# Kernel optimization log

Hardware: AMD Instinct MI355X
Metric: run time of the kernel (lower is better)

## Reference

```python
import jax, jax.numpy as jnp
import numpy as np

EMB = 64
L = 2
NU = 100000
NI = 50000
ER = 1000000
ET = 800000
EP = 200000


def setup_inputs() -> dict:
    key = jax.random.key(0)
    ks = jax.random.split(key, 32)
    f = jnp.float32
    def nrm(k, shape, s=0.01):
        return (jax.random.normal(k, shape) * s).astype(f)
    inp = {}
    # graph structure (int)
    inp['rate_src'] = jax.random.randint(ks[0], (ER,), 0, NU)
    inp['rate_dst'] = jax.random.randint(ks[1], (ER,), 0, NI)
    inp['trust_src'] = jax.random.randint(ks[2], (ET,), 0, NU)
    inp['trust_dst'] = jax.random.randint(ks[3], (ET,), 0, NU)
    inp['pos_u'] = jax.random.randint(ks[4], (EP,), 0, NU)
    inp['pos_i'] = jax.random.randint(ks[5], (EP,), 0, NI)
    inp['neg_u'] = jax.random.randint(ks[6], (EP,), 0, NU)
    inp['neg_i'] = jax.random.randint(ks[7], (EP,), 0, NI)
    # embeddings (init normal(0, 0.01) per init_weights)
    inp['eu'] = nrm(ks[8], (NU, EMB))
    inp['ei'] = nrm(ks[9], (NI, EMB))
    # per-rel GATv2 params, stacked over L layers; [:,0]=fc_src, [:,1]=fc_dst
    inp['rate_W'] = nrm(ks[10], (L, 2, EMB, EMB))
    inp['rate_b'] = jnp.zeros((L, 2, EMB), f)
    inp['rate_attn'] = nrm(ks[11], (L, EMB), 0.1)
    inp['rate_bias'] = jnp.zeros((L, EMB), f)
    inp['rb_W'] = nrm(ks[12], (L, 2, EMB, EMB))
    inp['rb_b'] = jnp.zeros((L, 2, EMB), f)
    inp['rb_attn'] = nrm(ks[13], (L, EMB), 0.1)
    inp['rb_bias'] = jnp.zeros((L, EMB), f)
    inp['tr_W'] = nrm(ks[14], (L, 2, EMB, EMB))
    inp['tr_b'] = jnp.zeros((L, 2, EMB), f)
    inp['tr_attn'] = nrm(ks[15], (L, EMB), 0.1)
    inp['tr_bias'] = jnp.zeros((L, EMB), f)
    # attention-gate MLPs: [:, 0]=influence, [:, 1]=interest
    inp['attW1'] = nrm(ks[16], (L, 2, 2 * EMB, 2 * EMB))
    inp['attb1'] = jnp.zeros((L, 2, 2 * EMB), f)
    inp['attW2'] = nrm(ks[17], (L, 2, 2 * EMB))
    inp['attb2'] = jnp.zeros((L, 2), f)
    return inp


def gatv2(hs, hd, src, dst, Ws, bs, Wd, bd, attn, bias, n_dst):
    # DGL GATv2Conv, num_heads=1: e = attn . leaky_relu(Ws h_u + Wd h_v), slope 0.2
    fs = hs @ Ws + bs          # [Ns, E]
    fd = hd @ Wd + bd          # [Nd, E]
    e = jax.nn.leaky_relu(fs[src] + fd[dst], 0.2) @ attn  # [E]
    m = jax.ops.segment_max(e, dst, num_segments=n_dst)
    ex = jnp.exp(e - m[dst])
    denom = jax.ops.segment_sum(ex, dst, num_segments=n_dst)
    alpha = ex / denom[dst]
    out = jax.ops.segment_sum(alpha[:, None] * fs[src], dst, num_segments=n_dst)
    return out + bias


def _bn1(x):
    # BatchNorm1d(1), training-mode batch stats, affine identity at init
    mu = jnp.mean(x)
    var = jnp.mean((x - mu) ** 2)
    return (x - mu) * jax.lax.rsqrt(var + 1e-5)


def reference(eu, ei, rate_W, rate_b, rate_attn, rate_bias, rb_W, rb_b, rb_attn,
              rb_bias, tr_W, tr_b, tr_attn, tr_bias, attW1, attb1, attW2, attb2,
              rate_src, rate_dst, trust_src, trust_dst, pos_u, pos_i, neg_u, neg_i):
    n_users, n_items = eu.shape[0], ei.shape[0]
    hu, hi = eu, ei
    res_u, res_i = [eu], [ei]
    for l in range(rate_W.shape[0]):
        # interest diffusion: rate (user->item) and rated-by (item->user, reverse edges)
        hi_new = gatv2(hu, hi, rate_src, rate_dst, rate_W[l, 0], rate_b[l, 0],
                       rate_W[l, 1], rate_b[l, 1], rate_attn[l], rate_bias[l], n_items) + hi
        q = gatv2(hi, hu, rate_dst, rate_src, rb_W[l, 0], rb_b[l, 0],
                  rb_W[l, 1], rb_b[l, 1], rb_attn[l], rb_bias[l], n_users)
        # influence diffusion: trust (user->user)
        p = gatv2(hu, hu, trust_src, trust_dst, tr_W[l, 0], tr_b[l, 0],
                  tr_W[l, 1], tr_b[l, 1], tr_attn[l], tr_bias[l], n_users)
        def att(h2, i):
            z = (h2 @ attW1[l, i] + attb1[l, i]) @ attW2[l, i] + attb2[l, i]  # [N]
            return jax.nn.leaky_relu(_bn1(z), 0.01)
        a_inf = att(jnp.concatenate([hu, p], axis=1), 0)
        a_int = att(jnp.concatenate([hu, q], axis=1), 1)
        gamma = jax.nn.softmax(jnp.stack([a_inf, a_int], axis=1), axis=1)  # [N,2]
        hu = gamma[:, 0:1] * p + gamma[:, 1:2] * q + hu
        hi = hi_new
        res_u.append(hu)
        res_i.append(hi)
    hu_all = jnp.concatenate(res_u, axis=1)  # [NU, EMB*(1+L)]
    hi_all = jnp.concatenate(res_i, axis=1)
    pos = jnp.sum(hu_all[pos_u] * hi_all[pos_i], axis=1, keepdims=True)  # [EP,1]
    neg = jnp.sum(hu_all[neg_u] * hi_all[neg_i], axis=1, keepdims=True)
    return pos, neg
```

## Files before the change

kernel.cpp:

```cpp
#include <hip/hip_runtime.h>
#include <hip/hip_bf16.h>
#include <hip/hip_fp16.h>
#include <cstdint>

typedef __hip_bfloat16 bf16;
typedef __attribute__((ext_vector_type(8))) short frag_ab;
typedef __attribute__((ext_vector_type(4))) float frag_cd;
typedef __attribute__((ext_vector_type(4))) short short4v;
typedef __attribute__((ext_vector_type(8))) short short8v;
typedef unsigned short u16;

#define CAPA 56
#define CAPB 40
#define CAPC 32

__device__ __forceinline__ float b2f(short s){
  return __uint_as_float(((unsigned)(unsigned short)s) << 16);
}
__device__ __forceinline__ float h2f(short s){
  __half h; __builtin_memcpy(&h, &s, 2); return __half2float(h);
}
__device__ __forceinline__ short f2h_s(float x){
  __half h = __float2half(x);
  short s; __builtin_memcpy(&s, &h, 2); return s;
}
__device__ __forceinline__ void bf_split(float x, short& hi, short& lo){
  bf16 h = __float2bfloat16(x);
  float hf = __bfloat162float(h);
  bf16 l = __float2bfloat16(x - hf);
  __builtin_memcpy(&hi, &h, 2);
  __builtin_memcpy(&lo, &l, 2);
}

__device__ __forceinline__ float wave_sum(float v){
#pragma unroll
  for (int o = 32; o > 0; o >>= 1) v += __shfl_down(v, o, 64);
  return v;
}

__global__ void k_wsplit(const float* __restrict__ rateW, const float* __restrict__ rbW,
                         const float* __restrict__ trW,
                         short* __restrict__ Whi, short* __restrict__ Wlo){
  int tid = blockIdx.x * 256 + threadIdx.x;
  if (tid >= 12 * 4096) return;
  int m = tid >> 12, rem = tid & 4095;
  int lane = rem >> 6, rem2 = rem & 63;
  int pair = rem2 >> 3, j = rem2 & 7;
  int c = pair >> 1, h = pair & 1;
  int rel = m >> 2, li = m & 3;
  const float* base = (rel == 0) ? rateW : (rel == 1) ? rbW : trW;
  float v = base[(size_t)li * 4096 + (32 * h + (lane >> 4) * 8 + j) * 64 + 16 * c + (lane & 15)];
  short sh, sl; bf_split(v, sh, sl);
  Whi[tid] = sh; Wlo[tid] = sl;
}

__device__ __forceinline__ void dev_linear(int rowb, int nloc, int gofs, int nglob,
    const float* __restrict__ x, int xs, int xo,
    const short* __restrict__ Whi, const short* __restrict__ Wlo, int mcount,
    int m0, int m1, int m2, int m3,
    const float* b0, const float* b1, const float* b2, const float* b3,
    bf16* o0, bf16* o1, bf16* o2, bf16* o3){
  int lane = threadIdx.x & 63, w = threadIdx.x >> 6;
  int quad = lane >> 4, n16 = lane & 15;
  int rowbase = rowb + w * 16;
  if (rowbase >= nloc) return;
  int lrow = rowbase + n16; if (lrow >= nloc) lrow = nloc - 1;
  const float* xp = x + (size_t)lrow * xs + xo;
  frag_ab ahi[2], alo[2];
#pragma unroll
  for (int h = 0; h < 2; ++h){
    frag_ab vh, vl;
#pragma unroll
    for (int j = 0; j < 8; ++j){
      float xv = xp[32 * h + quad * 8 + j];
      short sh, sl; bf_split(xv, sh, sl);
      vh[j] = sh; vl[j] = sl;
    }
    ahi[h] = vh; alo[h] = vl;
  }
  int ms[4] = {m0, m1, m2, m3};
  const float* bs[4] = {b0, b1, b2, b3};
  bf16* os[4] = {o0, o1, o2, o3};
  for (int i = 0; i < mcount; ++i){
    const frag_ab* Bh = (const frag_ab*)(Whi + (size_t)ms[i] * 4096 + lane * 64);
    const frag_ab* Bl = (const frag_ab*)(Wlo + (size_t)ms[i] * 4096 + lane * 64);
    frag_cd acc[4];
#pragma unroll
    for (int c = 0; c < 4; ++c) acc[c] = frag_cd{0.f, 0.f, 0.f, 0.f};
#pragma unroll
    for (int c = 0; c < 4; ++c)
#pragma unroll
      for (int h = 0; h < 2; ++h){
        frag_ab bh = Bh[c * 2 + h], bl = Bl[c * 2 + h];
        acc[c] = __builtin_amdgcn_mfma_f32_16x16x32_bf16(ahi[h], bh, acc[c], 0, 0, 0);
        acc[c] = __builtin_amdgcn_mfma_f32_16x16x32_bf16(alo[h], bh, acc[c], 0, 0, 0);
        acc[c] = __builtin_amdgcn_mfma_f32_16x16x32_bf16(ahi[h], bl, acc[c], 0, 0, 0);
      }
    const float* bb = bs[i];
    bf16* oo = os[i];
#pragma unroll
    for (int reg = 0; reg < 4; ++reg){
      int r = rowbase + quad * 4 + reg;
      if (r >= nloc || gofs + r >= nglob) continue;
#pragma unroll
      for (int c = 0; c < 4; ++c)
        oo[(size_t)(gofs + r) * 64 + 16 * c + n16] = __float2bfloat16(acc[c][reg] + bb[16 * c + n16]);
    }
  }
}

struct LinArgs {
  int nblk; const float* x; int xs, xo, n, mcount;
  int m0, m1, m2, m3;
  const float *b0, *b1, *b2, *b3;
  bf16 *o0, *o1, *o2, *o3;
};
struct PrepArgs {
  int NBH, NBC, ER, ET, NU, NI;
  const int *rate_src, *rate_dst, *trust_src, *trust_dst;
  int *cntA, *cntB, *cntC;
  int *csrA; u16 *csrB; int *csrC;
  const float *eu, *ei;
  float *hu01, *hi_all;
  const short *Whi, *Wlo;
  LinArgs LU, LI;
  const float *W1, *b1v, *W2, *b2v;
  float *vvec, *cs;
};

__global__ void k_prep(PrepArgs a){
  int b = blockIdx.x, t = threadIdx.x;
  if (b < a.NBH){
    int k = b * 256 + t;
    if (k < a.ER){
      int s = a.rate_src[k], d = a.rate_dst[k];
      int pa = atomicAdd(a.cntA + d, 1);
      if (pa < CAPA) a.csrA[(size_t)d * CAPA + pa] = s;
      int pb = atomicAdd(a.cntB + s, 1);
      if (pb < CAPB) a.csrB[(size_t)s * CAPB + pb] = (u16)d;
    }
    if (k < a.ET){
      int s = a.trust_src[k], d = a.trust_dst[k];
      int pc = atomicAdd(a.cntC + d, 1);
      if (pc < CAPC) a.csrC[(size_t)d * CAPC + pc] = s;
    }
    return;
  }
  b -= a.NBH;
  if (b < a.LU.nblk){
    dev_linear(b * 64, a.LU.n, 0, a.LU.n, a.LU.x, a.LU.xs, a.LU.xo, a.Whi, a.Wlo,
               a.LU.mcount, a.LU.m0, a.LU.m1, a.LU.m2, a.LU.m3,
               a.LU.b0, a.LU.b1, a.LU.b2, a.LU.b3, a.LU.o0, a.LU.o1, a.LU.o2, a.LU.o3);
    return;
  }
  b -= a.LU.nblk;
  if (b < a.LI.nblk){
    dev_linear(b * 64, a.LI.n, 0, a.LI.n, a.LI.x, a.LI.xs, a.LI.xo, a.Whi, a.Wlo,
               a.LI.mcount, a.LI.m0, a.LI.m1, a.LI.m2, a.LI.m3,
               a.LI.b0, a.LI.b1, a.LI.b2, a.LI.b3, a.LI.o0, a.LI.o1, a.LI.o2, a.LI.o3);
    return;
  }
  b -= a.LI.nblk;
  if (b < a.NBC){
    int tot = (a.NU + a.NI) * 16;
    int tu = a.NU * 16;
    int base = b * 1024 + t;
#pragma unroll
    for (int s = 0; s < 4; ++s){
      int idx = base + s * 256;
      if (idx >= tot) break;
      if (idx < tu){
        int r = idx >> 4, jj = idx & 15;
        *(float4*)(a.hu01 + (size_t)r * 128 + 4 * jj) =
            *(const float4*)(a.eu + (size_t)r * 64 + 4 * jj);
      } else {
        int t2 = idx - tu;
        int r = t2 >> 4, jj = t2 & 15;
        *(float4*)(a.hi_all + (size_t)r * 192 + 4 * jj) =
            *(const float4*)(a.ei + (size_t)r * 64 + 4 * jj);
      }
    }
    return;
  }
  for (int it = t; it < 512; it += 256){
    int li = it >> 7, r = it & 127;
    float acc = 0.f;
    for (int c = 0; c < 128; ++c)
      acc += a.W1[(size_t)(li * 128 + r) * 128 + c] * a.W2[li * 128 + c];
    a.vvec[li * 128 + r] = acc;
    if (r == 0){
      float cacc = a.b2v[li];
      for (int c = 0; c < 128; ++c)
        cacc += a.b1v[li * 128 + c] * a.W2[li * 128 + c];
      a.cs[li] = cacc;
    }
  }
}

struct GatArgs {
  int nblk, n, cap, of16;
  const int *cnt;
  const int *csr; const u16 *csr16;
  const bf16 *fs, *fd;
  const float *attn, *bias;
  void *out; int os, oo;
  const float *res; int rs, ro;
};

__device__ __forceinline__ void dev_gat(int lb, const GatArgs& g){
  int d = lb * 4 + (threadIdx.x >> 6);
  if (d >= g.n) return;
  int lane = threadIdx.x & 63;
  int gg = lane >> 3, l8 = lane & 7;
  short8v dv = *(const short8v*)(g.fd + (size_t)d * 64 + 8 * l8);
  float fdv[8];
#pragma unroll
  for (int j = 0; j < 8; ++j) fdv[j] = b2f(dv[j]);
  float4 a0 = *(const float4*)(g.attn + 8 * l8);
  float4 a1 = *(const float4*)(g.attn + 8 * l8 + 4);
  float a8[8] = {a0.x, a0.y, a0.z, a0.w, a1.x, a1.y, a1.z, a1.w};
  float acc[8];
#pragma unroll
  for (int j = 0; j < 8; ++j) acc[j] = 0.f;
  float den = 0.f;
  int c = g.cnt[d]; if (c > g.cap) c = g.cap;
  size_t base = (size_t)d * g.cap;
  for (int idx = 0; idx < c; idx += 8){
    int e = idx + gg;
    bool valid = e < c;
    size_t ei = base + (valid ? e : idx);
    int s = g.csr16 ? (int)g.csr16[ei] : g.csr[ei];
    short8v sv = *(const short8v*)(g.fs + (size_t)s * 64 + 8 * l8);
    float f[8];
    float tt = 0.f;
#pragma unroll
    for (int j = 0; j < 8; ++j){
      f[j] = b2f(sv[j]);
      float v = f[j] + fdv[j];
      v = (v > 0.f) ? v : 0.2f * v;
      tt += v * a8[j];
    }
#pragma unroll
    for (int o = 1; o < 8; o <<= 1) tt += __shfl_xor(tt, o, 64);
    float ex = valid ? __expf(tt) : 0.f;
#pragma unroll
    for (int j = 0; j < 8; ++j) acc[j] += ex * f[j];
    den += ex;
  }
#pragma unroll
  for (int o = 8; o < 64; o <<= 1){
#pragma unroll
    for (int j = 0; j < 8; ++j) acc[j] += __shfl_xor(acc[j], o, 64);
    den += __shfl_xor(den, o, 64);
  }
  if (gg == 0){
    float inv = (den > 0.f) ? 1.f / den : 0.f;
    float4 b0 = *(const float4*)(g.bias + 8 * l8);
    float4 b1 = *(const float4*)(g.bias + 8 * l8 + 4);
    float o8[8];
    o8[0] = acc[0] * inv + b0.x; o8[1] = acc[1] * inv + b0.y;
    o8[2] = acc[2] * inv + b0.z; o8[3] = acc[3] * inv + b0.w;
    o8[4] = acc[4] * inv + b1.x; o8[5] = acc[5] * inv + b1.y;
    o8[6] = acc[6] * inv + b1.z; o8[7] = acc[7] * inv + b1.w;
    if (g.res){
      float4 r0 = *(const float4*)(g.res + (size_t)d * g.rs + g.ro + 8 * l8);
      float4 r1 = *(const float4*)(g.res + (size_t)d * g.rs + g.ro + 8 * l8 + 4);
      o8[0] += r0.x; o8[1] += r0.y; o8[2] += r0.z; o8[3] += r0.w;
      o8[4] += r1.x; o8[5] += r1.y; o8[6] += r1.z; o8[7] += r1.w;
    }
    if (g.of16){
      short8v hv;
#pragma unroll
      for (int j = 0; j < 8; ++j) hv[j] = f2h_s(o8[j]);
      *(short8v*)((short*)g.out + (size_t)d * g.os + g.oo + 8 * l8) = hv;
    } else {
      float* op = (float*)g.out + (size_t)d * g.os + g.oo + 8 * l8;
      *(float4*)op = make_float4(o8[0], o8[1], o8[2], o8[3]);
      *(float4*)(op + 4) = make_float4(o8[4], o8[5], o8[6], o8[7]);
    }
  }
}

__global__ void k_gat3(GatArgs A, GatArgs B, GatArgs C){
  int b = blockIdx.x;
  if (b < A.nblk){ dev_gat(b, A); return; }
  b -= A.nblk;
  if (b < B.nblk){ dev_gat(b, B); return; }
  b -= B.nblk;
  dev_gat(b, C);
}

struct GzArgs {
  int nbz, NU, l;
  const float* hu01;
  const __half* pf16;
  const __half* q;
  const float *vvec, *cs;
  float *z1, *z2, *bsums;
  const short *Whi, *Wlo;
  LinArgs LI;
};

__global__ void k_gatez(GzArgs a){
  int b = blockIdx.x;
  if (b >= a.nbz){
    int blk = b - a.nbz;
    dev_linear(blk * 64, a.LI.n, 0, a.LI.n, a.LI.x, a.LI.xs, a.LI.xo, a.Whi, a.Wlo,
               a.LI.mcount, a.LI.m0, a.LI.m1, a.LI.m2, a.LI.m3,
               a.LI.b0, a.LI.b1, a.LI.b2, a.LI.b3, a.LI.o0, a.LI.o1, a.LI.o2, a.LI.o3);
    return;
  }
  __shared__ float part[4][4];
  int w = threadIdx.x >> 6, j = threadIdx.x & 63;
  int nidx = b * 4 + w;
  float lz1 = 0.f, lz2 = 0.f;
  if (nidx < a.NU){
    const float* v1 = a.vvec + a.l * 256;
    const float* v2 = a.vvec + a.l * 256 + 128;
    float h  = a.hu01[(size_t)nidx * 128 + a.l * 64 + j];
    float pv = a.pf16 ? h2f(((const short*)a.pf16)[(size_t)nidx * 64 + j])
                      : a.hu01[(size_t)nidx * 128 + 64 + j];
    float qv = h2f(((const short*)a.q)[(size_t)nidx * 64 + j]);
    float t1 = wave_sum(h * v1[j] + pv * v1[64 + j]);
    float t2 = wave_sum(h * v2[j] + qv * v2[64 + j]);
    if (j == 0){
      lz1 = t1 + a.cs[a.l * 2 + 0];
      lz2 = t2 + a.cs[a.l * 2 + 1];
      a.z1[nidx] = lz1;
      a.z2[nidx] = lz2;
    }
  }
  if (j == 0){
    part[w][0] = lz1; part[w][1] = lz1 * lz1;
    part[w][2] = lz2; part[w][3] = lz2 * lz2;
  }
  __syncthreads();
  if (threadIdx.x < 4)
    a.bsums[(size_t)b * 4 + threadIdx.x] =
        part[0][threadIdx.x] + part[1][threadIdx.x] +
        part[2][threadIdx.x] + part[3][threadIdx.x];
}

__global__ void k_bn(const float* __restrict__ bsums, int nb,
                     double* __restrict__ gpart, double* __restrict__ sums,
                     int* __restrict__ tick){
  __shared__ double sh[256];
  __shared__ int lastflag;
  int c = threadIdx.x & 3, r0 = blockIdx.x * 64 + (threadIdx.x >> 2);
  double acc = 0.0;
  for (int i = r0; i < nb; i += gridDim.x * 64)
    acc += (double)bsums[(size_t)i * 4 + c];
  sh[threadIdx.x] = acc;
  __syncthreads();
  for (int s = 128; s >= 4; s >>= 1){
    if (threadIdx.x < s) sh[threadIdx.x] += sh[threadIdx.x + s];
    __syncthreads();
  }
  if (threadIdx.x < 4) gpart[(size_t)blockIdx.x * 4 + threadIdx.x] = sh[threadIdx.x];
  __threadfence();
  if (threadIdx.x == 0) lastflag = (atomicAdd(tick, 1) == (int)gridDim.x - 1);
  __syncthreads();
  if (lastflag){
    __threadfence();
    int k0 = threadIdx.x >> 2;
    double a2 = 0.0;
    for (int i = k0; i < (int)gridDim.x; i += 64) a2 += gpart[(size_t)i * 4 + c];
    sh[threadIdx.x] = a2;
    __syncthreads();
    for (int s = 128; s >= 4; s >>= 1){
      if (threadIdx.x < s) sh[threadIdx.x] += sh[threadIdx.x + s];
      __syncthreads();
    }
    if (threadIdx.x < 4) sums[threadIdx.x] = sh[threadIdx.x];
  }
}

struct CmbArgs {
  int l, NU;
  float* hu01; __half* hu2; const __half* q;
  const float *z1, *z2; const double* sums;
  int dolin;
  const short *Whi, *Wlo;
  int m0, m1, m2, m3;
  const float *b0, *b1, *b2, *b3;
  bf16 *o0, *o1, *o2, *o3;
};

__global__ void k_combine(CmbArgs a){
  __shared__ float lds[64][65];
  int r0 = blockIdx.x * 64;
  int t = threadIdx.x;
  double invn = 1.0 / (double)a.NU;
  double mu1 = a.sums[0] * invn, mu2 = a.sums[2] * invn;
  float var1 = (float)(a.sums[1] * invn - mu1 * mu1);
  float var2 = (float)(a.sums[3] * invn - mu2 * mu2);
  float rs1 = rsqrtf(var1 + 1e-5f), rs2 = rsqrtf(var2 + 1e-5f);
  int nloc = a.NU - r0; if (nloc > 64) nloc = 64;
#pragma unroll
  for (int s = 0; s < 16; ++s){
    int elem = s * 256 + t;
    int row = elem >> 6, col = elem & 63;
    if (row < nloc){
      int r = r0 + row;
      float a1 = (a.z1[r] - (float)mu1) * rs1;
      float a2 = (a.z2[r] - (float)mu2) * rs2;
      a1 = a1 > 0.f ? a1 : 0.01f * a1;
      a2 = a2 > 0.f ? a2 : 0.01f * a2;
      float mx = fmaxf(a1, a2);
      float e1 = __expf(a1 - mx), e2 = __expf(a2 - mx);
      float inv = 1.f / (e1 + e2);
      float pv = (a.l == 0) ? a.hu01[(size_t)r * 128 + 64 + col]
                            : h2f(((const short*)a.hu2)[(size_t)r * 64 + col]);
      float qv = h2f(((const short*)a.q)[(size_t)r * 64 + col]);
      float h  = a.hu01[(size_t)r * 128 + a.l * 64 + col];
      float out = e1 * inv * pv + e2 * inv * qv + h;
      if (a.l == 0){
        a.hu01[(size_t)r * 128 + 64 + col] = out;
        lds[row][col] = out;
      } else {
        ((short*)a.hu2)[(size_t)r * 64 + col] = f2h_s(out);
      }
    }
  }
  if (!a.dolin) return;
  __syncthreads();
  dev_linear(0, nloc, r0, a.NU, &lds[0][0], 65, 0, a.Whi, a.Wlo, 4,
             a.m0, a.m1, a.m2, a.m3, a.b0, a.b1, a.b2, a.b3,
             a.o0, a.o1, a.o2, a.o3);
}

__global__ void k_score(const int* __restrict__ pu, const int* __restrict__ pi,
                        const int* __restrict__ nu, const int* __restrict__ ni,
                        const float* __restrict__ hu01, const __half* __restrict__ hu2,
                        const float* __restrict__ hi_all,
                        float* __restrict__ out, int EP){
  int gw = blockIdx.x * 4 + (threadIdx.x >> 6);
  int sub = (threadIdx.x >> 4) & 3, l16 = threadIdx.x & 15;
  int k = gw * 4 + sub;
  if (k >= 2 * EP) return;
  int u, i;
  if (k < EP){ u = pu[k]; i = pi[k]; } else { u = nu[k - EP]; i = ni[k - EP]; }
  const float4* A = (const float4*)(hu01 + (size_t)u * 128);
  const float4* B = (const float4*)(hi_all + (size_t)i * 192);
  float acc = 0.f;
#pragma unroll
  for (int t = 0; t < 2; ++t){
    float4 av = A[l16 + 16 * t];
    float4 bv = B[l16 + 16 * t];
    acc += av.x * bv.x + av.y * bv.y + av.z * bv.z + av.w * bv.w;
  }
  short4v hv = *(const short4v*)((const short*)hu2 + (size_t)u * 64 + 4 * l16);
  float4 b2v = B[l16 + 32];
  acc += h2f(hv[0]) * b2v.x + h2f(hv[1]) * b2v.y + h2f(hv[2]) * b2v.z + h2f(hv[3]) * b2v.w;
#pragma unroll
  for (int o = 8; o > 0; o >>= 1) acc += __shfl_xor(acc, o, 64);
  if (l16 == 0) out[k] = acc;
}

extern "C" void kernel_launch(void* const* d_in, const int* in_sizes, int n_in,
                              void* d_out, int out_size, void* d_ws, size_t ws_size,
                              hipStream_t stream) {
  const int*   rate_src  = (const int*)  d_in[0];
  const int*   rate_dst  = (const int*)  d_in[1];
  const int*   trust_src = (const int*)  d_in[2];
  const int*   trust_dst = (const int*)  d_in[3];
  const int*   pos_u     = (const int*)  d_in[4];
  const int*   pos_i     = (const int*)  d_in[5];
  const int*   neg_u     = (const int*)  d_in[6];
  const int*   neg_i     = (const int*)  d_in[7];
  const float* eu        = (const float*)d_in[8];
  const float* ei        = (const float*)d_in[9];
  const float* rate_W    = (const float*)d_in[10];
  const float* rate_b    = (const float*)d_in[11];
  const float* rate_attn = (const float*)d_in[12];
  const float* rate_bias = (const float*)d_in[13];
  const float* rb_W      = (const float*)d_in[14];
  const float* rb_b      = (const float*)d_in[15];
  const float* rb_attn   = (const float*)d_in[16];
  const float* rb_bias   = (const float*)d_in[17];
  const float* tr_W      = (const float*)d_in[18];
  const float* tr_b      = (const float*)d_in[19];
  const float* tr_attn   = (const float*)d_in[20];
  const float* tr_bias   = (const float*)d_in[21];
  const float* attW1     = (const float*)d_in[22];
  const float* attb1     = (const float*)d_in[23];
  const float* attW2     = (const float*)d_in[24];
  const float* attb2     = (const float*)d_in[25];

  const int ER = in_sizes[0];
  const int ET = in_sizes[2];
  const int EP = in_sizes[4];
  const int NU = in_sizes[8] / 64;
  const int NI = in_sizes[9] / 64;
  const int EM = (ER > ET) ? ER : ET;

  float*  ws     = (float*)d_ws;
  float*  hu01   = ws;
  float*  hi_all = hu01 + (size_t)NU * 128;
  bf16*   fdA    = (bf16*)(hi_all + (size_t)NI * 192);
  bf16*   fsB    = fdA + (size_t)NI * 64;
  __half* hu2    = (__half*)(fsB + (size_t)NI * 64);
  __half* qf     = hu2 + (size_t)NU * 64;
  bf16*   tb     = (bf16*)(qf + (size_t)NU * 64);
  bf16*   fsA    = tb;
  bf16*   fdB    = tb + (size_t)NU * 64;
  bf16*   fsC    = tb + (size_t)NU * 128;
  bf16*   fdC    = tb + (size_t)NU * 192;
  float*  z1     = (float*)(tb + (size_t)NU * 256);
  float*  z2     = z1 + NU;
  float*  bsums  = z2 + NU;
  float*  vvec   = bsums + (size_t)(((NU + 3) / 4) * 4);
  float*  cs     = vvec + 512;
  double* sums   = (double*)(((uintptr_t)(cs + 4) + 15) & ~(uintptr_t)15);
  double* gpart  = sums + 4;
  short*  Whi    = (short*)(gpart + 512);
  short*  Wlo    = Whi + 12 * 4096;
  int*    cntA   = (int*)(Wlo + 12 * 4096);
  int*    cntB   = cntA + NI;
  int*    cntC   = cntB + NU;
  int*    tick   = cntC + NU;
  int*    csrA   = tick + 8;
  u16*    csrB   = (u16*)(csrA + (size_t)NI * CAPA);
  int*    csrC   = (int*)(csrB + (size_t)NU * CAPB);

  auto cdiv = [](int a, int b){ return (a + b - 1) / b; };
  const int nbz = cdiv(NU, 4);

  hipMemsetAsync(cntA, 0, (size_t)(NI + 2 * NU + 8) * 4, stream);
  k_wsplit<<<192, 256, 0, stream>>>(rate_W, rb_W, tr_W, Whi, Wlo);

  PrepArgs pa;
  pa.NBH = cdiv(EM, 256);
  pa.NBC = cdiv((NU + NI) * 16, 1024);
  pa.ER = ER; pa.ET = ET; pa.NU = NU; pa.NI = NI;
  pa.rate_src = rate_src; pa.rate_dst = rate_dst;
  pa.trust_src = trust_src; pa.trust_dst = trust_dst;
  pa.cntA = cntA; pa.cntB = cntB; pa.cntC = cntC;
  pa.csrA = csrA; pa.csrB = csrB; pa.csrC = csrC;
  pa.eu = eu; pa.ei = ei; pa.hu01 = hu01; pa.hi_all = hi_all;
  pa.Whi = Whi; pa.Wlo = Wlo;
  pa.LU.nblk = cdiv(NU, 64); pa.LU.x = eu; pa.LU.xs = 64; pa.LU.xo = 0;
  pa.LU.n = NU; pa.LU.mcount = 4;
  pa.LU.m0 = 0; pa.LU.m1 = 5; pa.LU.m2 = 8; pa.LU.m3 = 9;
  pa.LU.b0 = rate_b + 0;  pa.LU.b1 = rb_b + 64;
  pa.LU.b2 = tr_b + 0;    pa.LU.b3 = tr_b + 64;
  pa.LU.o0 = fsA; pa.LU.o1 = fdB; pa.LU.o2 = fsC; pa.LU.o3 = fdC;
  pa.LI.nblk = cdiv(NI, 64); pa.LI.x = ei; pa.LI.xs = 64; pa.LI.xo = 0;
  pa.LI.n = NI; pa.LI.mcount = 2;
  pa.LI.m0 = 1; pa.LI.m1 = 4; pa.LI.m2 = 0; pa.LI.m3 = 0;
  pa.LI.b0 = rate_b + 64; pa.LI.b1 = rb_b + 0;
  pa.LI.b2 = nullptr; pa.LI.b3 = nullptr;
  pa.LI.o0 = fdA; pa.LI.o1 = fsB; pa.LI.o2 = nullptr; pa.LI.o3 = nullptr;
  pa.W1 = attW1; pa.b1v = attb1; pa.W2 = attW2; pa.b2v = attb2;
  pa.vvec = vvec; pa.cs = cs;
  k_prep<<<pa.NBH + pa.LU.nblk + pa.LI.nblk + pa.NBC + 1, 256, 0, stream>>>(pa);

  for (int l = 0; l < 2; ++l){
    GatArgs A, B, C;
    A.nblk = cdiv(NI, 4); A.n = NI; A.cap = CAPA; A.of16 = 0;
    A.cnt = cntA; A.csr = csrA; A.csr16 = nullptr; A.fs = fsA; A.fd = fdA;
    A.attn = rate_attn + l * 64; A.bias = rate_bias + l * 64;
    A.out = hi_all; A.os = 192; A.oo = (l + 1) * 64;
    A.res = hi_all; A.rs = 192; A.ro = l * 64;
    B.nblk = cdiv(NU, 4); B.n = NU; B.cap = CAPB; B.of16 = 1;
    B.cnt = cntB; B.csr = nullptr; B.csr16 = csrB; B.fs = fsB; B.fd = fdB;
    B.attn = rb_attn + l * 64; B.bias = rb_bias + l * 64;
    B.out = qf; B.os = 64; B.oo = 0;
    B.res = nullptr; B.rs = 0; B.ro = 0;
    C.nblk = cdiv(NU, 4); C.n = NU; C.cap = CAPC;
    C.cnt = cntC; C.csr = csrC; C.csr16 = nullptr; C.fs = fsC; C.fd = fdC;
    C.attn = tr_attn + l * 64; C.bias = tr_bias + l * 64;
    if (l == 0){ C.of16 = 0; C.out = hu01; C.os = 128; C.oo = 64; }
    else       { C.of16 = 1; C.out = hu2;  C.os = 64;  C.oo = 0;  }
    C.res = nullptr; C.rs = 0; C.ro = 0;
    k_gat3<<<A.nblk + B.nblk + C.nblk, 256, 0, stream>>>(A, B, C);

    GzArgs gz;
    gz.nbz = nbz; gz.NU = NU; gz.l = l;
    gz.hu01 = hu01; gz.pf16 = (l == 0) ? nullptr : hu2; gz.q = qf;
    gz.vvec = vvec; gz.cs = cs; gz.z1 = z1; gz.z2 = z2; gz.bsums = bsums;
    gz.Whi = Whi; gz.Wlo = Wlo;
    if (l == 0){
      gz.LI.nblk = cdiv(NI, 64); gz.LI.x = hi_all; gz.LI.xs = 192; gz.LI.xo = 64;
      gz.LI.n = NI; gz.LI.mcount = 2;
      gz.LI.m0 = 3; gz.LI.m1 = 6; gz.LI.m2 = 0; gz.LI.m3 = 0;
      gz.LI.b0 = rate_b + 192; gz.LI.b1 = rb_b + 128;
      gz.LI.b2 = nullptr; gz.LI.b3 = nullptr;
      gz.LI.o0 = fdA; gz.LI.o1 = fsB; gz.LI.o2 = nullptr; gz.LI.o3 = nullptr;
    } else {
      gz.LI.nblk = 0; gz.LI.x = nullptr; gz.LI.xs = 0; gz.LI.xo = 0;
      gz.LI.n = 0; gz.LI.mcount = 0;
      gz.LI.m0 = gz.LI.m1 = gz.LI.m2 = gz.LI.m3 = 0;
      gz.LI.b0 = gz.LI.b1 = gz.LI.b2 = gz.LI.b3 = nullptr;
      gz.LI.o0 = gz.LI.o1 = gz.LI.o2 = gz.LI.o3 = nullptr;
    }
    k_gatez<<<nbz + gz.LI.nblk, 256, 0, stream>>>(gz);

    k_bn<<<128, 256, 0, stream>>>(bsums, nbz, gpart, sums, tick + l);

    CmbArgs cm;
    cm.l = l; cm.NU = NU;
    cm.hu01 = hu01; cm.hu2 = hu2; cm.q = qf;
    cm.z1 = z1; cm.z2 = z2; cm.sums = sums;
    cm.dolin = (l == 0) ? 1 : 0;
    cm.Whi = Whi; cm.Wlo = Wlo;
    cm.m0 = 2; cm.m1 = 7; cm.m2 = 10; cm.m3 = 11;
    cm.b0 = rate_b + 128; cm.b1 = rb_b + 192;
    cm.b2 = tr_b + 128;   cm.b3 = tr_b + 192;
    cm.o0 = fsA; cm.o1 = fdB; cm.o2 = fsC; cm.o3 = fdC;
    k_combine<<<cdiv(NU, 64), 256, 0, stream>>>(cm);
  }

  k_score<<<cdiv(2 * EP, 16), 256, 0, stream>>>(pos_u, pos_i, neg_u, neg_i,
      hu01, hu2, hi_all, (float*)d_out, EP);
}
```

Baseline: 954.0 us.

## Split CSR build into count and fill passes, prefetch GAT gathers, store fp16 item layer

```diff
diff --git a/kernel.cpp b/kernel.cpp
--- a/kernel.cpp
+++ b/kernel.cpp
@@ -117,11 +117,11 @@
 };
 struct PrepArgs {
   int NBH, NBC, ER, ET, NU, NI;
-  const int *rate_src, *rate_dst, *trust_src, *trust_dst;
+  const int *rate_src, *rate_dst, *trust_dst;
   int *cntA, *cntB, *cntC;
-  int *csrA; u16 *csrB; int *csrC;
+  u16 *posA, *posB, *posC;
   const float *eu, *ei;
-  float *hu01, *hi_all;
+  float *hu01, *hi01;
   const short *Whi, *Wlo;
   LinArgs LU, LI;
   const float *W1, *b1v, *W2, *b2v;
@@ -133,16 +133,12 @@
   if (b < a.NBH){
     int k = b * 256 + t;
     if (k < a.ER){
-      int s = a.rate_src[k], d = a.rate_dst[k];
-      int pa = atomicAdd(a.cntA + d, 1);
-      if (pa < CAPA) a.csrA[(size_t)d * CAPA + pa] = s;
-      int pb = atomicAdd(a.cntB + s, 1);
-      if (pb < CAPB) a.csrB[(size_t)s * CAPB + pb] = (u16)d;
+      int d = a.rate_dst[k], s = a.rate_src[k];
+      a.posA[k] = (u16)atomicAdd(a.cntA + d, 1);
+      a.posB[k] = (u16)atomicAdd(a.cntB + s, 1);
     }
     if (k < a.ET){
-      int s = a.trust_src[k], d = a.trust_dst[k];
-      int pc = atomicAdd(a.cntC + d, 1);
-      if (pc < CAPC) a.csrC[(size_t)d * CAPC + pc] = s;
+      a.posC[k] = (u16)atomicAdd(a.cntC + a.trust_dst[k], 1);
     }
     return;
   }
@@ -176,7 +172,7 @@
       } else {
         int t2 = idx - tu;
         int r = t2 >> 4, jj = t2 & 15;
-        *(float4*)(a.hi_all + (size_t)r * 192 + 4 * jj) =
+        *(float4*)(a.hi01 + (size_t)r * 128 + 4 * jj) =
             *(const float4*)(a.ei + (size_t)r * 64 + 4 * jj);
       }
     }
@@ -197,6 +193,25 @@
   }
 }
 
+__global__ void k_fill(const int* __restrict__ rs_, const int* __restrict__ rd_,
+                       const int* __restrict__ ts_, const int* __restrict__ td_,
+                       const u16* __restrict__ posA, const u16* __restrict__ posB,
+                       const u16* __restrict__ posC,
+                       int* __restrict__ csrA, u16* __restrict__ csrB,
+                       int* __restrict__ csrC, int ER, int ET){
+  int k = blockIdx.x * 256 + threadIdx.x;
+  if (k < ER){
+    int s = rs_[k], d = rd_[k];
+    int pa = posA[k], pb = posB[k];
+    if (pa < CAPA) csrA[(size_t)d * CAPA + pa] = s;
+    if (pb < CAPB) csrB[(size_t)s * CAPB + pb] = (u16)d;
+  }
+  if (k < ET){
+    int pc = posC[k];
+    if (pc < CAPC) csrC[(size_t)td_[k] * CAPC + pc] = ts_[k];
+  }
+}
+
 struct GatArgs {
   int nblk, n, cap, of16;
   const int *cnt;
@@ -212,6 +227,10 @@
   if (d >= g.n) return;
   int lane = threadIdx.x & 63;
   int gg = lane >> 3, l8 = lane & 7;
+  int c = g.cnt[d]; if (c > g.cap) c = g.cap;
+  size_t base = (size_t)d * g.cap;
+  int my_s = 0;
+  if (lane < c) my_s = g.csr16 ? (int)g.csr16[base + lane] : g.csr[base + lane];
   short8v dv = *(const short8v*)(g.fd + (size_t)d * 64 + 8 * l8);
   float fdv[8];
 #pragma unroll
@@ -223,14 +242,16 @@
 #pragma unroll
   for (int j = 0; j < 8; ++j) acc[j] = 0.f;
   float den = 0.f;
-  int c = g.cnt[d]; if (c > g.cap) c = g.cap;
-  size_t base = (size_t)d * g.cap;
+  int s_cur = __shfl(my_s, gg, 64);
+  short8v sv = *(const short8v*)(g.fs + (size_t)s_cur * 64 + 8 * l8);
   for (int idx = 0; idx < c; idx += 8){
-    int e = idx + gg;
-    bool valid = e < c;
-    size_t ei = base + (valid ? e : idx);
-    int s = g.csr16 ? (int)g.csr16[ei] : g.csr[ei];
-    short8v sv = *(const short8v*)(g.fs + (size_t)s * 64 + 8 * l8);
+    short8v svn = sv;
+    int nn = idx + 8;
+    if (nn < c){
+      int s_nxt = __shfl(my_s, nn + gg, 64);
+      svn = *(const short8v*)(g.fs + (size_t)s_nxt * 64 + 8 * l8);
+    }
+    bool valid = (idx + gg) < c;
     float f[8];
     float tt = 0.f;
 #pragma unroll
@@ -246,6 +267,7 @@
 #pragma unroll
     for (int j = 0; j < 8; ++j) acc[j] += ex * f[j];
     den += ex;
+    sv = svn;
   }
 #pragma unroll
   for (int o = 8; o < 64; o <<= 1){
@@ -432,7 +454,7 @@
 __global__ void k_score(const int* __restrict__ pu, const int* __restrict__ pi,
                         const int* __restrict__ nu, const int* __restrict__ ni,
                         const float* __restrict__ hu01, const __half* __restrict__ hu2,
-                        const float* __restrict__ hi_all,
+                        const float* __restrict__ hi01, const __half* __restrict__ hi2,
                         float* __restrict__ out, int EP){
   int gw = blockIdx.x * 4 + (threadIdx.x >> 6);
   int sub = (threadIdx.x >> 4) & 3, l16 = threadIdx.x & 15;
@@ -441,7 +463,7 @@
   int u, i;
   if (k < EP){ u = pu[k]; i = pi[k]; } else { u = nu[k - EP]; i = ni[k - EP]; }
   const float4* A = (const float4*)(hu01 + (size_t)u * 128);
-  const float4* B = (const float4*)(hi_all + (size_t)i * 192);
+  const float4* B = (const float4*)(hi01 + (size_t)i * 128);
   float acc = 0.f;
 #pragma unroll
   for (int t = 0; t < 2; ++t){
@@ -449,9 +471,10 @@
     float4 bv = B[l16 + 16 * t];
     acc += av.x * bv.x + av.y * bv.y + av.z * bv.z + av.w * bv.w;
   }
-  short4v hv = *(const short4v*)((const short*)hu2 + (size_t)u * 64 + 4 * l16);
-  float4 b2v = B[l16 + 32];
-  acc += h2f(hv[0]) * b2v.x + h2f(hv[1]) * b2v.y + h2f(hv[2]) * b2v.z + h2f(hv[3]) * b2v.w;
+  short4v ha = *(const short4v*)((const short*)hu2 + (size_t)u * 64 + 4 * l16);
+  short4v hb = *(const short4v*)((const short*)hi2 + (size_t)i * 64 + 4 * l16);
+  acc += h2f(ha[0]) * h2f(hb[0]) + h2f(ha[1]) * h2f(hb[1])
+       + h2f(ha[2]) * h2f(hb[2]) + h2f(ha[3]) * h2f(hb[3]);
 #pragma unroll
   for (int o = 8; o > 0; o >>= 1) acc += __shfl_xor(acc, o, 64);
   if (l16 == 0) out[k] = acc;
@@ -494,14 +517,18 @@
   const int NI = in_sizes[9] / 64;
   const int EM = (ER > ET) ? ER : ET;
 
-  float*  ws     = (float*)d_ws;
-  float*  hu01   = ws;
-  float*  hi_all = hu01 + (size_t)NU * 128;
-  bf16*   fdA    = (bf16*)(hi_all + (size_t)NI * 192);
+  float*  wsp    = (float*)d_ws;
+  float*  hu01   = wsp;
+  float*  hi01   = hu01 + (size_t)NU * 128;
+  __half* hi2    = (__half*)(hi01 + (size_t)NI * 128);
+  __half* hu2    = hi2 + (size_t)NI * 64;
+  __half* qf     = hu2 + (size_t)NU * 64;
+  u16*    posA   = (u16*)qf;
+  u16*    posB   = posA + ER;
+  u16*    posC   = posB + ER;
+  bf16*   fdA    = (bf16*)(qf + (size_t)NU * 64);
   bf16*   fsB    = fdA + (size_t)NI * 64;
-  __half* hu2    = (__half*)(fsB + (size_t)NI * 64);
-  __half* qf     = hu2 + (size_t)NU * 64;
-  bf16*   tb     = (bf16*)(qf + (size_t)NU * 64);
+  bf16*   tb     = fsB + (size_t)NI * 64;
   bf16*   fsA    = tb;
   bf16*   fdB    = tb + (size_t)NU * 64;
   bf16*   fsC    = tb + (size_t)NU * 128;
@@ -533,11 +560,10 @@
   pa.NBH = cdiv(EM, 256);
   pa.NBC = cdiv((NU + NI) * 16, 1024);
   pa.ER = ER; pa.ET = ET; pa.NU = NU; pa.NI = NI;
-  pa.rate_src = rate_src; pa.rate_dst = rate_dst;
-  pa.trust_src = trust_src; pa.trust_dst = trust_dst;
+  pa.rate_src = rate_src; pa.rate_dst = rate_dst; pa.trust_dst = trust_dst;
   pa.cntA = cntA; pa.cntB = cntB; pa.cntC = cntC;
-  pa.csrA = csrA; pa.csrB = csrB; pa.csrC = csrC;
-  pa.eu = eu; pa.ei = ei; pa.hu01 = hu01; pa.hi_all = hi_all;
+  pa.posA = posA; pa.posB = posB; pa.posC = posC;
+  pa.eu = eu; pa.ei = ei; pa.hu01 = hu01; pa.hi01 = hi01;
   pa.Whi = Whi; pa.Wlo = Wlo;
   pa.LU.nblk = cdiv(NU, 64); pa.LU.x = eu; pa.LU.xs = 64; pa.LU.xo = 0;
   pa.LU.n = NU; pa.LU.mcount = 4;
@@ -555,13 +581,18 @@
   pa.vvec = vvec; pa.cs = cs;
   k_prep<<<pa.NBH + pa.LU.nblk + pa.LI.nblk + pa.NBC + 1, 256, 0, stream>>>(pa);
 
+  k_fill<<<cdiv(EM, 256), 256, 0, stream>>>(rate_src, rate_dst, trust_src, trust_dst,
+      posA, posB, posC, csrA, csrB, csrC, ER, ET);
+
   for (int l = 0; l < 2; ++l){
     GatArgs A, B, C;
-    A.nblk = cdiv(NI, 4); A.n = NI; A.cap = CAPA; A.of16 = 0;
+    A.nblk = cdiv(NI, 4); A.n = NI; A.cap = CAPA;
     A.cnt = cntA; A.csr = csrA; A.csr16 = nullptr; A.fs = fsA; A.fd = fdA;
     A.attn = rate_attn + l * 64; A.bias = rate_bias + l * 64;
-    A.out = hi_all; A.os = 192; A.oo = (l + 1) * 64;
-    A.res = hi_all; A.rs = 192; A.ro = l * 64;
+    if (l == 0){ A.of16 = 0; A.out = hi01; A.os = 128; A.oo = 64;
+                 A.res = hi01; A.rs = 128; A.ro = 0; }
+    else       { A.of16 = 1; A.out = hi2;  A.os = 64;  A.oo = 0;
+                 A.res = hi01; A.rs = 128; A.ro = 64; }
     B.nblk = cdiv(NU, 4); B.n = NU; B.cap = CAPB; B.of16 = 1;
     B.cnt = cntB; B.csr = nullptr; B.csr16 = csrB; B.fs = fsB; B.fd = fdB;
     B.attn = rb_attn + l * 64; B.bias = rb_bias + l * 64;
@@ -581,7 +612,7 @@
     gz.vvec = vvec; gz.cs = cs; gz.z1 = z1; gz.z2 = z2; gz.bsums = bsums;
     gz.Whi = Whi; gz.Wlo = Wlo;
     if (l == 0){
-      gz.LI.nblk = cdiv(NI, 64); gz.LI.x = hi_all; gz.LI.xs = 192; gz.LI.xo = 64;
+      gz.LI.nblk = cdiv(NI, 64); gz.LI.x = hi01; gz.LI.xs = 128; gz.LI.xo = 64;
       gz.LI.n = NI; gz.LI.mcount = 2;
       gz.LI.m0 = 3; gz.LI.m1 = 6; gz.LI.m2 = 0; gz.LI.m3 = 0;
       gz.LI.b0 = rate_b + 192; gz.LI.b1 = rb_b + 128;
@@ -612,5 +643,5 @@
   }
 
   k_score<<<cdiv(2 * EP, 16), 256, 0, stream>>>(pos_u, pos_i, neg_u, neg_i,
-      hu01, hu2, hi_all, (float*)d_out, EP);
-}
+      hu01, hu2, hi01, hi2, (float*)d_out, EP);
+}
```

After: 882.4 us. -7.5%, faster.
